# Kernel tuning notes

Measured on AMD Instinct MI355X. Metric: run time of the kernel, lower is better.

The kernel has to match this reference:

```python
import jax, jax.numpy as jnp
import numpy as np

EPS = 1e-5

def conv1x1(x, w):
    # x: (B,C,H,W), w: (O,C) -> (B,O,H,W)
    return jnp.einsum('bchw,oc->bohw', x, w)

def bn_relu(y, g, b, m, v):
    s = g / jnp.sqrt(v + EPS)
    return jax.nn.relu(y * s[None, :, None, None] + (b - m * s)[None, :, None, None])

def cbr(x, w, g, b, m, v):
    return bn_relu(conv1x1(x, w), g, b, m, v)

def _bn_params(key, c):
    k1, k2, k3, k4 = jax.random.split(key, 4)
    g = 1.0 + 0.1 * jax.random.normal(k1, (c,), jnp.float32)
    b = 0.1 * jax.random.normal(k2, (c,), jnp.float32)
    m = 0.05 * jax.random.normal(k3, (c,), jnp.float32)
    v = jax.random.uniform(k4, (c,), jnp.float32, 0.5, 1.5)
    return g, b, m, v

def setup_inputs() -> dict:
    key = jax.random.key(0)
    B, Cin, H, W = 8, 512, 64, 64
    Ck, Cv, Cout = 256, 256, 512
    ks = jax.random.split(key, 12)
    def w(k, o, c):
        return jax.random.normal(k, (o, c), jnp.float32) * (1.0 / np.sqrt(c))
    inp = {}
    inp['x'] = jax.random.normal(ks[0], (B, Cin, H, W), jnp.float32)
    # f_key
    inp['kW1'] = w(ks[1], Ck, Cin); inp['kG1'], inp['kB1'], inp['kM1'], inp['kV1'] = _bn_params(ks[2], Ck)
    inp['kW2'] = w(ks[3], Ck, Ck);  inp['kG2'], inp['kB2'], inp['kM2'], inp['kV2'] = _bn_params(ks[4], Ck)
    # f_query
    inp['qW1'] = w(ks[5], Ck, Cin); inp['qG1'], inp['qB1'], inp['qM1'], inp['qV1'] = _bn_params(ks[6], Ck)
    inp['qW2'] = w(ks[7], Ck, Ck);  inp['qG2'], inp['qB2'], inp['qM2'], inp['qV2'] = _bn_params(ks[8], Ck)
    # f_value
    inp['vW'] = w(ks[9], Cv, Cin)
    # W (output projection)
    inp['wW'] = w(ks[10], Cout, Cv); inp['wG'], inp['wB'], inp['wM'], inp['wV'] = _bn_params(ks[11], Cout)
    return inp

def reference(x,
              kW1, kG1, kB1, kM1, kV1, kW2, kG2, kB2, kM2, kV2,
              qW1, qG1, qB1, qM1, qV1, qW2, qG2, qB2, qM2, qV2,
              vW,
              wW, wG, wB, wM, wV):
    B, _, H, W = x.shape
    q = cbr(cbr(x, qW1, qG1, qB1, qM1, qV1), qW2, qG2, qB2, qM2, qV2)  # (B,Ck,H,W)
    k = cbr(cbr(x, kW1, kG1, kB1, kM1, kV1), kW2, kG2, kB2, kM2, kV2)  # (B,Ck,H,W)
    v = conv1x1(x, vW)                                                  # (B,Cv,H,W)
    Ck = q.shape[1]; Cv = v.shape[1]; N = H * W
    qf = q.reshape(B, Ck, N)   # query = qf^T -> (B,N,Ck)
    kf = k.reshape(B, Ck, N)
    vf = v.reshape(B, Cv, N)
    sim = jnp.einsum('bcn,bcm->bnm', qf, kf) * (Ck ** -0.5)  # (B,N,N)
    attn = jax.nn.softmax(sim, axis=-1)
    ctx = jnp.einsum('bnm,bcm->bcn', attn, vf).reshape(B, Cv, H, W)
    return cbr(ctx, wW, wG, wB, wM, wV)
```

## Files before the change

kernel.cpp:

```cpp
#include <hip/hip_runtime.h>
#include <hip/hip_bf16.h>

typedef __attribute__((ext_vector_type(8))) short bf16x8;
typedef __attribute__((ext_vector_type(4))) float f32x4;

#define MFMA16(a, b, c) __builtin_amdgcn_mfma_f32_16x16x32_bf16(a, b, c, 0, 0, 0)

static __device__ __forceinline__ unsigned short f2bf(float f) {
  union { __hip_bfloat16 h; unsigned short u; } cv;
  cv.h = __float2bfloat16(f);
  return cv.u;
}

static __device__ __forceinline__ void gload16(const void* gptr, void* lptr) {
  __builtin_amdgcn_global_load_lds(
      (const __attribute__((address_space(1))) void*)gptr,
      (__attribute__((address_space(3))) void*)lptr, 16, 0, 0);
}


__global__ void conv_w_k(const float* __restrict__ qW1, const float* __restrict__ kW1,
                         const float* __restrict__ qW2, const float* __restrict__ kW2,
                         const float* __restrict__ vW, const float* __restrict__ wW,
                         __hip_bfloat16* __restrict__ dst) {
  int i = blockIdx.x * 256 + threadIdx.x;
  const float* src; int off;
  if (i < 131072)      { src = qW1; off = i; }
  else if (i < 262144) { src = kW1; off = i - 131072; }
  else if (i < 327680) { src = qW2; off = i - 262144; }
  else if (i < 393216) { src = kW2; off = i - 327680; }
  else if (i < 524288) { src = vW;  off = i - 393216; }
  else                 { src = wW;  off = i - 524288; }
  dst[i] = __float2bfloat16(src[off]);
}

__global__ void bn_all_k(const float* __restrict__ qG1, const float* __restrict__ qB1, const float* __restrict__ qM1, const float* __restrict__ qV1,
                         const float* __restrict__ qG2, const float* __restrict__ qB2, const float* __restrict__ qM2, const float* __restrict__ qV2,
                         const float* __restrict__ kG1, const float* __restrict__ kB1, const float* __restrict__ kM1, const float* __restrict__ kV1,
                         const float* __restrict__ kG2, const float* __restrict__ kB2, const float* __restrict__ kM2, const float* __restrict__ kV2,
                         const float* __restrict__ wG, const float* __restrict__ wB, const float* __restrict__ wM, const float* __restrict__ wV,
                         float* __restrict__ base) {
  int bidx = blockIdx.x, tid = threadIdx.x;
  const float *g, *b, *m, *v; float *s, *t; int i;
  if (bidx == 0)      { g = qG1; b = qB1; m = qM1; v = qV1; s = base;        t = base + 256;  i = tid; }
  else if (bidx == 1) { g = qG2; b = qB2; m = qM2; v = qV2; s = base + 512;  t = base + 768;  i = tid; }
  else if (bidx == 2) { g = kG1; b = kB1; m = kM1; v = kV1; s = base + 1024; t = base + 1280; i = tid; }
  else if (bidx == 3) { g = kG2; b = kB2; m = kM2; v = kV2; s = base + 1536; t = base + 1792; i = tid; }
  else                { g = wG;  b = wB;  m = wM;  v = wV;  s = base + 2048; t = base + 2560; i = (bidx - 4) * 256 + tid; }
  float sv = g[i] * rsqrtf(v[i] + 1e-5f);
  s[i] = sv;
  t[i] = b[i] - m[i] * sv;
}

__global__ __launch_bounds__(256) void transpose_k(const float* __restrict__ x,
                                                   __hip_bfloat16* __restrict__ xT) {
  __shared__ float tile[64][65];
  const int n0 = blockIdx.x * 64, c0 = blockIdx.y * 64, b = blockIdx.z;
  const int tx = threadIdx.x, ty = threadIdx.y;
  const float* xp = x + ((size_t)(b * 512 + c0) * 4096) + n0;
#pragma unroll
  for (int i = 0; i < 16; ++i) {
    int c = ty + 4 * i;
    tile[c][tx] = xp[(size_t)c * 4096 + tx];
  }
  __syncthreads();
  __hip_bfloat16* op = xT + ((size_t)(b * 4096 + n0) * 512) + c0;
#pragma unroll
  for (int i = 0; i < 16; ++i) {
    int nl = ty + 4 * i;
    op[(size_t)nl * 512 + tx] = __float2bfloat16(tile[tx][nl]);
  }
}

template <int EPI>
__global__ __launch_bounds__(256) void gemm_nt_k(
    const __hip_bfloat16* __restrict__ A, long sA,
    const __hip_bfloat16* __restrict__ B, long sB,
    void* __restrict__ Cp, long sC,
    int lda, int ldb, int ldc, int K,
    const float* __restrict__ s, const float* __restrict__ t) {
  __shared__ short As[128][72];
  __shared__ short Bs[128][72];
  const int tid = threadIdx.x;
  const int w = tid >> 6, l = tid & 63, g = l >> 4, ln = l & 15;
  const int wr = w >> 1, wc = w & 1;
  const int rb = blockIdx.x * 128, cb = blockIdx.y * 128;
  const __hip_bfloat16* Ab = A + (size_t)blockIdx.z * sA;
  const __hip_bfloat16* Bb = B + (size_t)blockIdx.z * sB;

  f32x4 acc[4][4];
#pragma unroll
  for (int i = 0; i < 4; ++i)
#pragma unroll
    for (int j = 0; j < 4; ++j) acc[i][j] = (f32x4){0.f, 0.f, 0.f, 0.f};

  const int r0 = tid >> 3;
  const int c8 = (tid & 7) * 8;

  for (int k0 = 0; k0 < K; k0 += 64) {
#pragma unroll
    for (int i = 0; i < 4; ++i) {
      const int r = r0 + 32 * i;
      *(uint4*)&As[r][c8] = *(const uint4*)(Ab + (size_t)(rb + r) * lda + (k0 + c8));
      *(uint4*)&Bs[r][c8] = *(const uint4*)(Bb + (size_t)(cb + r) * ldb + (k0 + c8));
    }
    __syncthreads();
#pragma unroll
    for (int kk = 0; kk < 2; ++kk) {
      bf16x8 av[4], bv[4];
#pragma unroll
      for (int i = 0; i < 4; ++i) av[i] = *(const bf16x8*)&As[64 * wr + 16 * i + ln][32 * kk + 8 * g];
#pragma unroll
      for (int i = 0; i < 4; ++i) bv[i] = *(const bf16x8*)&Bs[64 * wc + 16 * i + ln][32 * kk + 8 * g];
#pragma unroll
      for (int mi = 0; mi < 4; ++mi)
#pragma unroll
        for (int ni = 0; ni < 4; ++ni)
          acc[mi][ni] = MFMA16(av[mi], bv[ni], acc[mi][ni]);
    }
    __syncthreads();
  }

  const int row0 = rb + 64 * wr + 4 * g;
  const int col0 = cb + 64 * wc + ln;

  if (EPI == 2) {
    float* C = (float*)Cp + (size_t)blockIdx.z * sC;
#pragma unroll
    for (int mi = 0; mi < 4; ++mi) {
#pragma unroll
      for (int r = 0; r < 4; ++r) {
        const int R = row0 + 16 * mi + r;
        const float sr = s[R], tr = t[R];
#pragma unroll
        for (int ni = 0; ni < 4; ++ni) {
          float v = fmaf(acc[mi][ni][r], sr, tr);
          C[(size_t)R * ldc + (col0 + 16 * ni)] = v > 0.f ? v : 0.f;
        }
      }
    }
  } else {
    __hip_bfloat16* C = (__hip_bfloat16*)Cp + (size_t)blockIdx.z * sC;
    float sc[4], tc[4];
    if (EPI == 1) {
#pragma unroll
      for (int ni = 0; ni < 4; ++ni) { sc[ni] = s[col0 + 16 * ni]; tc[ni] = t[col0 + 16 * ni]; }
    }
#pragma unroll
    for (int mi = 0; mi < 4; ++mi) {
#pragma unroll
      for (int ni = 0; ni < 4; ++ni) {
#pragma unroll
        for (int r = 0; r < 4; ++r) {
          float v = acc[mi][ni][r];
          if (EPI == 1) { v = fmaf(v, sc[ni], tc[ni]); v = v > 0.f ? v : 0.f; }
          C[(size_t)(row0 + 16 * mi + r) * ldc + (col0 + 16 * ni)] = __float2bfloat16(v);
        }
      }
    }
  }
}

__global__ __launch_bounds__(256, 2) void flash_k(
    const __hip_bfloat16* __restrict__ Q,
    const __hip_bfloat16* __restrict__ Kt,
    const __hip_bfloat16* __restrict__ V,
    __hip_bfloat16* __restrict__ O) {
  __shared__ short Ks[2][64 * 256];
  __shared__ short Ps[64 * 64];
  __shared__ float aLds[64];
  __shared__ float lLds[64];
  __shared__ int fLds[4];

  const int tid = threadIdx.x;
  const int w = tid >> 6, l = tid & 63, g = l >> 4, ln = l & 15;
  const int bid = blockIdx.x;
  const int batch = bid & 7;
  const int qb = (bid >> 3) << 6;
  const size_t bo = (size_t)batch * (4096 * 256);
  const float CE = 0.09016844005556021f;

  const int swz45 = (16 * g) ^ ((ln & 3) << 4);
  const int s6 = ((ln >> 2) & 1) << 6;
  const char* Ka0 = (const char*)Ks[0] + (ln * 512 + swz45 + s6);
  const char* Ka1 = Ka0 + (((ln >> 2) & 1) ? -64 : 64);
  const char* Kb0 = Ka0 + 32768;
  const char* Kb1 = Ka1 + 32768;
  const char* Pr0 = (const char*)Ps + (ln * 128 + swz45 + s6);
  const char* Pr1 = Pr0 + (((ln >> 2) & 1) ? -64 : 64);
  const int pwOff = (16 * w + ln) * 128 + 8 * (g & 1) + (((g >> 1) ^ (ln & 1)) << 4) +
                    (((ln >> 1) & 1) << 5) + s6;

  bf16x8 qf[8];
  {
    const __hip_bfloat16* qp = Q + bo + (size_t)(qb + 16 * w + ln) * 256 + 8 * g;
#pragma unroll
    for (int kk = 0; kk < 8; ++kk) qf[kk] = *(const bf16x8*)(qp + 32 * kk);
  }

  f32x4 acc[4][4];
#pragma unroll
  for (int qg = 0; qg < 4; ++qg)
#pragma unroll
    for (int ci = 0; ci < 4; ++ci) acc[qg][ci] = (f32x4){0.f, 0.f, 0.f, 0.f};
  float m_run = -1e30f, l_run = 0.f;

  const int kRow = 16 * w + (l >> 5);
  const int kChunk = (l & 31) ^ (l >> 5);
  const short* kPtr[8];
#pragma unroll
  for (int j = 0; j < 8; ++j)
    kPtr[j] = (const short*)(Kt + bo) + (size_t)(kRow + 2 * j) * 256 + 8 * (kChunk ^ ((2 * j) & 7));
  const short* vPtr[4];
#pragma unroll
  for (int ci = 0; ci < 4; ++ci)
    vPtr[ci] = (const short*)(V + bo) + (size_t)(64 * w + 16 * ci + ln) * 4096 + 8 * g;

  bf16x8 vfrA[8], vfrB[8];

#define STAGEK(NB)                                                     \
  do {                                                                 \
    _Pragma("unroll") for (int j = 0; j < 8; ++j) {                    \
      gload16(kPtr[j], (short*)Ks[NB] + w * 4096 + j * 512);           \
      kPtr[j] += 16384;                      \
    }                                                                  \
  } while (0)

#define ISSUEV(VARR)                                                   \
  do {                                                                 \
    _Pragma("unroll") for (int ci = 0; ci < 4; ++ci) {                 \
      asm volatile("global_load_dwordx4 %0, %2, off\n\t"               \
                   "global_load_dwordx4 %1, %2, off offset:64"         \
                   : "=&v"(VARR[2 * ci]), "=&v"(VARR[2 * ci + 1])      \
                   : "v"(vPtr[ci]));                                   \
      vPtr[ci] += 64;                  \
    }                                                                  \
  } while (0)

  STAGEK(0);
  __builtin_amdgcn_sched_barrier(0);
  ISSUEV(vfrA);
  __builtin_amdgcn_sched_barrier(0);

#define BODY(T, K0P, K1P, VCUR, VNXT, NB)                                      \
  do {                                                                         \
                      \
    asm volatile("s_waitcnt vmcnt(8)" ::: "memory");                           \
    __builtin_amdgcn_sched_barrier(0);                                         \
                                    \
    f32x4 sf[4];                                                               \
    _Pragma("unroll") for (int mi = 0; mi < 4; ++mi)                           \
        sf[mi] = (f32x4){0.f, 0.f, 0.f, 0.f};                                  \
    __builtin_amdgcn_s_setprio(1);                                             \
    _Pragma("unroll") for (int kk = 0; kk < 8; ++kk) {                         \
      const char* kp = ((kk & 1) ? K1P : K0P) + 128 * (kk >> 1);               \
      _Pragma("unroll") for (int mi = 0; mi < 4; ++mi) {                       \
        bf16x8 a = *(const bf16x8*)(kp + 8192 * mi);                           \
        sf[mi] = MFMA16(a, qf[kk], sf[mi]);                                    \
      }                                                                        \
    }                                                                          \
    __builtin_amdgcn_s_setprio(0);                                             \
    __builtin_amdgcn_sched_barrier(0);                                         \
    if ((T) < 63) {                                                            \
      STAGEK(NB);                               \
      __builtin_amdgcn_sched_barrier(0);                                       \
      ISSUEV(VNXT);                           \
      __builtin_amdgcn_sched_barrier(0);                                       \
    }                                                                          \
                                          \
    float sv[16];                                                              \
    _Pragma("unroll") for (int mi = 0; mi < 4; ++mi)                           \
        _Pragma("unroll") for (int r = 0; r < 4; ++r)                          \
        sv[4 * mi + r] = sf[mi][r];                                            \
    float a0 = fmaxf(fmaxf(sv[0], sv[1]), sv[2]);                              \
    float a1 = fmaxf(fmaxf(sv[3], sv[4]), sv[5]);                              \
    float a2 = fmaxf(fmaxf(sv[6], sv[7]), sv[8]);                              \
    float a3 = fmaxf(fmaxf(sv[9], sv[10]), sv[11]);                            \
    float a4 = fmaxf(fmaxf(sv[12], sv[13]), sv[14]);                           \
    float mmax = fmaxf(fmaxf(fmaxf(fmaxf(a0, a1), a2), fmaxf(a3, a4)), sv[15]);\
    mmax = fmaxf(mmax, __shfl_xor(mmax, 16));                                  \
    mmax = fmaxf(mmax, __shfl_xor(mmax, 32));                                  \
    float alpha = 1.0f;                                                        \
    int rs = 0;                                                                \
    if (!__all((mmax - m_run) * CE <= 8.0f)) {                                 \
      float m_new = fmaxf(m_run, mmax);                                        \
      alpha = exp2f((m_run - m_new) * CE);                                     \
      l_run *= alpha;                                                          \
      m_run = m_new;                                                           \
      rs = 1;                                                                  \
    }                                                                          \
    float p[16], psum = 0.f;                                                   \
    _Pragma("unroll") for (int j = 0; j < 16; ++j) {                           \
      p[j] = exp2f((sv[j] - m_run) * CE);                                      \
      psum += p[j];                                                            \
    }                                                                          \
    psum += __shfl_xor(psum, 16);                                              \
    psum += __shfl_xor(psum, 32);                                              \
    l_run += psum;                                                             \
    {                                                                          \
      uint2 pk0, pk1, pk2, pk3;                                                \
      pk0.x = (unsigned)f2bf(p[0]) | ((unsigned)f2bf(p[1]) << 16);             \
      pk0.y = (unsigned)f2bf(p[2]) | ((unsigned)f2bf(p[3]) << 16);             \
      pk1.x = (unsigned)f2bf(p[4]) | ((unsigned)f2bf(p[5]) << 16);             \
      pk1.y = (unsigned)f2bf(p[6]) | ((unsigned)f2bf(p[7]) << 16);             \
      pk2.x = (unsigned)f2bf(p[8]) | ((unsigned)f2bf(p[9]) << 16);             \
      pk2.y = (unsigned)f2bf(p[10]) | ((unsigned)f2bf(p[11]) << 16);           \
      pk3.x = (unsigned)f2bf(p[12]) | ((unsigned)f2bf(p[13]) << 16);           \
      pk3.y = (unsigned)f2bf(p[14]) | ((unsigned)f2bf(p[15]) << 16);           \
      char* Pb = (char*)Ps;                                                    \
      *(uint2*)(Pb + (pwOff ^ 0)) = pk0;                                       \
      *(uint2*)(Pb + (pwOff ^ 32)) = pk1;                                      \
      *(uint2*)(Pb + (pwOff ^ 64)) = pk2;                                      \
      *(uint2*)(Pb + (pwOff ^ 96)) = pk3;                                      \
    }                                                                          \
    if (g == 0) aLds[16 * w + ln] = alpha;                                     \
    if (l == 0) fLds[w] = rs;                                                  \
                                  \
    asm volatile("s_waitcnt lgkmcnt(0)" ::: "memory");                         \
    __builtin_amdgcn_sched_barrier(0);                                         \
    __builtin_amdgcn_s_barrier();                                              \
    asm volatile("" ::: "memory");                                             \
    __builtin_amdgcn_sched_barrier(0);                                         \
                              \
    {                                                                          \
      int4 fl = *(const int4*)fLds;                                            \
      if (fl.x | fl.y | fl.z | fl.w) {                                         \
        _Pragma("unroll") for (int qg = 0; qg < 4; ++qg) {                     \
          f32x4 av = *(const f32x4*)&aLds[16 * qg + 4 * g];                    \
          _Pragma("unroll") for (int ci = 0; ci < 4; ++ci) acc[qg][ci] *= av;  \
        }                                                                      \
      }                                                                        \
    }                                                                          \
                         \
    if ((T) < 63) {                                                            \
      asm volatile("s_waitcnt vmcnt(16)" ::: "memory");                        \
    } else {                                                                   \
      asm volatile("s_waitcnt vmcnt(0)" ::: "memory");                         \
    }                                                                          \
    __builtin_amdgcn_sched_barrier(0);                                         \
                              \
    __builtin_amdgcn_s_setprio(1);                                             \
    _Pragma("unroll") for (int kk = 0; kk < 2; ++kk) {                         \
      _Pragma("unroll") for (int qg = 0; qg < 4; ++qg) {                       \
        bf16x8 pa = *(const bf16x8*)((kk ? Pr1 : Pr0) + 2048 * qg);            \
        _Pragma("unroll") for (int ci = 0; ci < 4; ++ci)                       \
            acc[qg][ci] = MFMA16(pa, VCUR[2 * ci + kk], acc[qg][ci]);          \
      }                                                                        \
    }                                                                          \
    __builtin_amdgcn_s_setprio(0);                                             \
    __builtin_amdgcn_sched_barrier(0);                                         \
                   \
    __builtin_amdgcn_s_barrier();                                              \
    asm volatile("" ::: "memory");                                             \
    __builtin_amdgcn_sched_barrier(0);                                         \
  } while (0)

  for (int tp = 0; tp < 32; ++tp) {
    const int t0 = 2 * tp;
    BODY(t0, Ka0, Ka1, vfrA, vfrB, 1);
    BODY(t0 + 1, Kb0, Kb1, vfrB, vfrA, 0);
  }
#undef BODY
#undef STAGEK
#undef ISSUEV

  if (g == 0) lLds[16 * w + ln] = l_run;
  __syncthreads();

  __hip_bfloat16* Ob = O + bo;
#pragma unroll
  for (int qg = 0; qg < 4; ++qg) {
    f32x4 lv = *(const f32x4*)&lLds[16 * qg + 4 * g];
    f32x4 li;
#pragma unroll
    for (int r = 0; r < 4; ++r) li[r] = 1.0f / lv[r];
#pragma unroll
    for (int ci = 0; ci < 4; ++ci) {
#pragma unroll
      for (int r = 0; r < 4; ++r) {
        float val = acc[qg][ci][r] * li[r];
        Ob[(size_t)(qb + 16 * qg + 4 * g + r) * 256 + 64 * w + 16 * ci + ln] = __float2bfloat16(val);
      }
    }
  }
}


extern "C" void kernel_launch(void* const* d_in, const int* in_sizes, int n_in,
                              void* d_out, int out_size, void* d_ws, size_t ws_size,
                              hipStream_t stream) {
  const float* x   = (const float*)d_in[0];
  const float* kW1 = (const float*)d_in[1];
  const float* kG1 = (const float*)d_in[2];
  const float* kB1 = (const float*)d_in[3];
  const float* kM1 = (const float*)d_in[4];
  const float* kV1 = (const float*)d_in[5];
  const float* kW2 = (const float*)d_in[6];
  const float* kG2 = (const float*)d_in[7];
  const float* kB2 = (const float*)d_in[8];
  const float* kM2 = (const float*)d_in[9];
  const float* kV2 = (const float*)d_in[10];
  const float* qW1 = (const float*)d_in[11];
  const float* qG1 = (const float*)d_in[12];
  const float* qB1 = (const float*)d_in[13];
  const float* qM1 = (const float*)d_in[14];
  const float* qV1 = (const float*)d_in[15];
  const float* qW2 = (const float*)d_in[16];
  const float* qG2 = (const float*)d_in[17];
  const float* qB2 = (const float*)d_in[18];
  const float* qM2 = (const float*)d_in[19];
  const float* qV2 = (const float*)d_in[20];
  const float* vW  = (const float*)d_in[21];
  const float* wW  = (const float*)d_in[22];
  const float* wG  = (const float*)d_in[23];
  const float* wB  = (const float*)d_in[24];
  const float* wM  = (const float*)d_in[25];
  const float* wV  = (const float*)d_in[26];

  char* ws = (char*)d_ws;
  __hip_bfloat16* bQW1 = (__hip_bfloat16*)(ws + 0);
  __hip_bfloat16* bKW1 = (__hip_bfloat16*)(ws + 262144);
  __hip_bfloat16* bQW2 = (__hip_bfloat16*)(ws + 524288);
  __hip_bfloat16* bKW2 = (__hip_bfloat16*)(ws + 655360);
  __hip_bfloat16* bVW  = (__hip_bfloat16*)(ws + 786432);
  __hip_bfloat16* bWW  = (__hip_bfloat16*)(ws + 1048576);
  float* bnBase = (float*)(ws + 1310720);
  float* sQ1 = bnBase + 0;
  float* tQ1 = bnBase + 256;
  float* sQ2 = bnBase + 512;
  float* tQ2 = bnBase + 768;
  float* sK1 = bnBase + 1024;
  float* tK1 = bnBase + 1280;
  float* sK2 = bnBase + 1536;
  float* tK2 = bnBase + 1792;
  float* sWo = bnBase + 2048;
  float* tWo = bnBase + 2560;
  __hip_bfloat16* xT   = (__hip_bfloat16*)(ws + 2097152);
  __hip_bfloat16* bufA = (__hip_bfloat16*)(ws + 35651584);
  __hip_bfloat16* q2b  = (__hip_bfloat16*)(ws + 52428800);
  __hip_bfloat16* k2b  = (__hip_bfloat16*)(ws + 69206016);
  __hip_bfloat16* vB   = (__hip_bfloat16*)(ws + 85983232);

  conv_w_k<<<2560, 256, 0, stream>>>(qW1, kW1, qW2, kW2, vW, wW, bQW1);
  bn_all_k<<<6, 256, 0, stream>>>(qG1, qB1, qM1, qV1, qG2, qB2, qM2, qV2,
                                  kG1, kB1, kM1, kV1, kG2, kB2, kM2, kV2,
                                  wG, wB, wM, wV, bnBase);

  transpose_k<<<dim3(64, 8, 8), dim3(64, 4), 0, stream>>>(x, xT);

  gemm_nt_k<1><<<dim3(32, 2, 8), 256, 0, stream>>>(xT, 2097152L, bQW1, 0L, bufA, 1048576L,
                                                   512, 512, 256, 512, sQ1, tQ1);
  gemm_nt_k<1><<<dim3(32, 2, 8), 256, 0, stream>>>(bufA, 1048576L, bQW2, 0L, q2b, 1048576L,
                                                   256, 256, 256, 256, sQ2, tQ2);
  gemm_nt_k<1><<<dim3(32, 2, 8), 256, 0, stream>>>(xT, 2097152L, bKW1, 0L, bufA, 1048576L,
                                                   512, 512, 256, 512, sK1, tK1);
  gemm_nt_k<1><<<dim3(32, 2, 8), 256, 0, stream>>>(bufA, 1048576L, bKW2, 0L, k2b, 1048576L,
                                                   256, 256, 256, 256, sK2, tK2);
  gemm_nt_k<0><<<dim3(2, 32, 8), 256, 0, stream>>>(bVW, 0L, xT, 2097152L, vB, 1048576L,
                                                   512, 512, 4096, 512, nullptr, nullptr);
  flash_k<<<512, 256, 0, stream>>>(q2b, k2b, vB, bufA);
  gemm_nt_k<2><<<dim3(4, 32, 8), 256, 0, stream>>>(bWW, 0L, bufA, 1048576L, d_out, 2097152L,
                                                   256, 256, 4096, 256, sWo, tWo);
}
```

Measured before the change: 367.8 us.

## Software-pipeline flash attention: overlap QK of next tile with PV of current

Restructures the attention main loop into a skewed pipeline. Each iteration computes QK^T for tile T while running the PV product for tile T-1, with explicit prologue and epilogue. The V register fragments drop from double to single buffering, and V loads are issued after PV so they overlap softmax. This aims to hide softmax and LDS latency behind MFMA work and to cut register pressure, but it changes the wait counts and barrier placement, which risks stalls.

Result: faster. 305.0 us (-17.1%).

```diff
diff --git a/kernel.cpp b/kernel.cpp
--- a/kernel.cpp
+++ b/kernel.cpp
@@ -182,10 +182,10 @@
 
   const int swz45 = (16 * g) ^ ((ln & 3) << 4);
   const int s6 = ((ln >> 2) & 1) << 6;
-  const char* Ka0 = (const char*)Ks[0] + (ln * 512 + swz45 + s6);
-  const char* Ka1 = Ka0 + (((ln >> 2) & 1) ? -64 : 64);
-  const char* Kb0 = Ka0 + 32768;
-  const char* Kb1 = Ka1 + 32768;
+  const char* KA0 = (const char*)Ks[0] + (ln * 512 + swz45 + s6);
+  const char* KA1 = KA0 + (((ln >> 2) & 1) ? -64 : 64);
+  const char* KB0 = KA0 + 32768;
+  const char* KB1 = KA1 + 32768;
   const char* Pr0 = (const char*)Ps + (ln * 128 + swz45 + s6);
   const char* Pr1 = Pr0 + (((ln >> 2) & 1) ? -64 : 64);
   const int pwOff = (16 * w + ln) * 128 + 8 * (g & 1) + (((g >> 1) ^ (ln & 1)) << 4) +
@@ -204,70 +204,76 @@
 #pragma unroll
     for (int ci = 0; ci < 4; ++ci) acc[qg][ci] = (f32x4){0.f, 0.f, 0.f, 0.f};
   float m_run = -1e30f, l_run = 0.f;
+  f32x4 sf[4];
+  bf16x8 vfr[8];
 
   const int kRow = 16 * w + (l >> 5);
   const int kChunk = (l & 31) ^ (l >> 5);
-  const short* kPtr[8];
-#pragma unroll
-  for (int j = 0; j < 8; ++j)
-    kPtr[j] = (const short*)(Kt + bo) + (size_t)(kRow + 2 * j) * 256 + 8 * (kChunk ^ ((2 * j) & 7));
-  const short* vPtr[4];
-#pragma unroll
-  for (int ci = 0; ci < 4; ++ci)
-    vPtr[ci] = (const short*)(V + bo) + (size_t)(64 * w + 16 * ci + ln) * 4096 + 8 * g;
-
-  bf16x8 vfrA[8], vfrB[8];
-
-#define STAGEK(NB)                                                     \
-  do {                                                                 \
-    _Pragma("unroll") for (int j = 0; j < 8; ++j) {                    \
-      gload16(kPtr[j], (short*)Ks[NB] + w * 4096 + j * 512);           \
-      kPtr[j] += 16384;                      \
-    }                                                                  \
-  } while (0)
-
-#define ISSUEV(VARR)                                                   \
-  do {                                                                 \
-    _Pragma("unroll") for (int ci = 0; ci < 4; ++ci) {                 \
-      asm volatile("global_load_dwordx4 %0, %2, off\n\t"               \
-                   "global_load_dwordx4 %1, %2, off offset:64"         \
-                   : "=&v"(VARR[2 * ci]), "=&v"(VARR[2 * ci + 1])      \
-                   : "v"(vPtr[ci]));                                   \
-      vPtr[ci] += 64;                  \
-    }                                                                  \
-  } while (0)
-
-  STAGEK(0);
-  __builtin_amdgcn_sched_barrier(0);
-  ISSUEV(vfrA);
-  __builtin_amdgcn_sched_barrier(0);
-
-#define BODY(T, K0P, K1P, VCUR, VNXT, NB)                                      \
-  do {                                                                         \
-                      \
-    asm volatile("s_waitcnt vmcnt(8)" ::: "memory");                           \
-    __builtin_amdgcn_sched_barrier(0);                                         \
-                                    \
-    f32x4 sf[4];                                                               \
+  const short* Kb = (const short*)(Kt + bo);
+  const short* Vp = (const short*)(V + bo) + (size_t)(64 * w + ln) * 4096 + 8 * g;
+
+#define SB __builtin_amdgcn_sched_barrier(0)
+
+#define STAGEK(NB, M0)                                                         \
+  do {                                                                         \
+    _Pragma("unroll") for (int j = 0; j < 8; ++j) {                            \
+      const short* gp =                                                        \
+          Kb + (size_t)((M0) + kRow + 2 * j) * 256 + 8 * (kChunk ^ ((2 * j) & 7)); \
+      gload16(gp, (short*)Ks[NB] + w * 4096 + j * 512);                        \
+    }                                                                          \
+  } while (0)
+
+#define ISSUEV(M0)                                                             \
+  do {                                                                         \
+    _Pragma("unroll") for (int ci = 0; ci < 4; ++ci)                           \
+        _Pragma("unroll") for (int kk = 0; kk < 2; ++kk) {                     \
+      const short* gp = Vp + (size_t)ci * (16 * 4096) + ((M0) + 32 * kk);      \
+      asm volatile("global_load_dwordx4 %0, %1, off"                           \
+                   : "=v"(vfr[2 * ci + kk]) : "v"(gp));                        \
+    }                                                                          \
+  } while (0)
+
+#define QKP(K0P, K1P)                                                          \
+  do {                                                                         \
     _Pragma("unroll") for (int mi = 0; mi < 4; ++mi)                           \
         sf[mi] = (f32x4){0.f, 0.f, 0.f, 0.f};                                  \
     __builtin_amdgcn_s_setprio(1);                                             \
     _Pragma("unroll") for (int kk = 0; kk < 8; ++kk) {                         \
-      const char* kp = ((kk & 1) ? K1P : K0P) + 128 * (kk >> 1);               \
+      const char* kp = ((kk & 1) ? (K1P) : (K0P)) + 128 * (kk >> 1);           \
       _Pragma("unroll") for (int mi = 0; mi < 4; ++mi) {                       \
         bf16x8 a = *(const bf16x8*)(kp + 8192 * mi);                           \
         sf[mi] = MFMA16(a, qf[kk], sf[mi]);                                    \
       }                                                                        \
     }                                                                          \
     __builtin_amdgcn_s_setprio(0);                                             \
-    __builtin_amdgcn_sched_barrier(0);                                         \
-    if ((T) < 63) {                                                            \
-      STAGEK(NB);                               \
-      __builtin_amdgcn_sched_barrier(0);                                       \
-      ISSUEV(VNXT);                           \
-      __builtin_amdgcn_sched_barrier(0);                                       \
-    }                                                                          \
-                                          \
+  } while (0)
+
+#define RESCALE                                                                \
+  do {                                                                         \
+    int4 fl = *(const int4*)fLds;                                              \
+    if (fl.x | fl.y | fl.z | fl.w) {                                           \
+      _Pragma("unroll") for (int qg = 0; qg < 4; ++qg) {                       \
+        f32x4 av = *(const f32x4*)&aLds[16 * qg + 4 * g];                      \
+        _Pragma("unroll") for (int ci = 0; ci < 4; ++ci) acc[qg][ci] *= av;    \
+      }                                                                        \
+    }                                                                          \
+  } while (0)
+
+#define PVP                                                                    \
+  do {                                                                         \
+    __builtin_amdgcn_s_setprio(1);                                             \
+    _Pragma("unroll") for (int kk = 0; kk < 2; ++kk) {                         \
+      _Pragma("unroll") for (int qg = 0; qg < 4; ++qg) {                       \
+        bf16x8 pa = *(const bf16x8*)((kk ? Pr1 : Pr0) + 2048 * qg);            \
+        _Pragma("unroll") for (int ci = 0; ci < 4; ++ci)                       \
+            acc[qg][ci] = MFMA16(pa, vfr[2 * ci + kk], acc[qg][ci]);           \
+      }                                                                        \
+    }                                                                          \
+    __builtin_amdgcn_s_setprio(0);                                             \
+  } while (0)
+
+#define SOFTMAX                                                                \
+  do {                                                                         \
     float sv[16];                                                              \
     _Pragma("unroll") for (int mi = 0; mi < 4; ++mi)                           \
         _Pragma("unroll") for (int r = 0; r < 4; ++r)                          \
@@ -315,54 +321,73 @@
     }                                                                          \
     if (g == 0) aLds[16 * w + ln] = alpha;                                     \
     if (l == 0) fLds[w] = rs;                                                  \
-                                  \
+  } while (0)
+
+#define BODY(K0P, K1P, NB, T, DOSTAGE)                                         \
+  do {                                                                         \
+    QKP(K0P, K1P);                                                             \
+    SB;                                                                        \
+    if (DOSTAGE) STAGEK(NB, ((T) + 1) << 6);                                   \
+    SB;                                                                        \
+    RESCALE;                                                                   \
+    if (DOSTAGE) { asm volatile("s_waitcnt vmcnt(8)" ::: "memory"); }          \
+    else         { asm volatile("s_waitcnt vmcnt(0)" ::: "memory"); }          \
+    SB;                                                                        \
+    PVP;                                                                       \
+    SB;                                                                        \
+    ISSUEV((T) << 6);                                                          \
+    SB;                                                                        \
     asm volatile("s_waitcnt lgkmcnt(0)" ::: "memory");                         \
-    __builtin_amdgcn_sched_barrier(0);                                         \
-    __builtin_amdgcn_s_barrier();                                              \
+    SB;                                                                        \
+    __builtin_amdgcn_s_barrier();                  \
     asm volatile("" ::: "memory");                                             \
-    __builtin_amdgcn_sched_barrier(0);                                         \
-                              \
-    {                                                                          \
-      int4 fl = *(const int4*)fLds;                                            \
-      if (fl.x | fl.y | fl.z | fl.w) {                                         \
-        _Pragma("unroll") for (int qg = 0; qg < 4; ++qg) {                     \
-          f32x4 av = *(const f32x4*)&aLds[16 * qg + 4 * g];                    \
-          _Pragma("unroll") for (int ci = 0; ci < 4; ++ci) acc[qg][ci] *= av;  \
-        }                                                                      \
-      }                                                                        \
-    }                                                                          \
-                         \
-    if ((T) < 63) {                                                            \
-      asm volatile("s_waitcnt vmcnt(16)" ::: "memory");                        \
-    } else {                                                                   \
-      asm volatile("s_waitcnt vmcnt(0)" ::: "memory");                         \
-    }                                                                          \
-    __builtin_amdgcn_sched_barrier(0);                                         \
-                              \
-    __builtin_amdgcn_s_setprio(1);                                             \
-    _Pragma("unroll") for (int kk = 0; kk < 2; ++kk) {                         \
-      _Pragma("unroll") for (int qg = 0; qg < 4; ++qg) {                       \
-        bf16x8 pa = *(const bf16x8*)((kk ? Pr1 : Pr0) + 2048 * qg);            \
-        _Pragma("unroll") for (int ci = 0; ci < 4; ++ci)                       \
-            acc[qg][ci] = MFMA16(pa, VCUR[2 * ci + kk], acc[qg][ci]);          \
-      }                                                                        \
-    }                                                                          \
-    __builtin_amdgcn_s_setprio(0);                                             \
-    __builtin_amdgcn_sched_barrier(0);                                         \
-                   \
-    __builtin_amdgcn_s_barrier();                                              \
+    SB;                                                                        \
+    SOFTMAX;                                                                   \
+    asm volatile("s_waitcnt vmcnt(8) lgkmcnt(0)" ::: "memory");                \
+    SB;                                                                        \
+    __builtin_amdgcn_s_barrier();          \
     asm volatile("" ::: "memory");                                             \
-    __builtin_amdgcn_sched_barrier(0);                                         \
-  } while (0)
-
-  for (int tp = 0; tp < 32; ++tp) {
-    const int t0 = 2 * tp;
-    BODY(t0, Ka0, Ka1, vfrA, vfrB, 1);
-    BODY(t0 + 1, Kb0, Kb1, vfrB, vfrA, 0);
-  }
+    SB;                                                                        \
+  } while (0)
+
+  STAGEK(0, 0);
+  SB;
+  asm volatile("s_waitcnt vmcnt(0)" ::: "memory");
+  SB;
+  __builtin_amdgcn_s_barrier();
+  asm volatile("" ::: "memory");
+  SB;
+  QKP(KA0, KA1);
+  SB;
+  STAGEK(1, 64);
+  SB;
+  ISSUEV(0);
+  SB;
+  SOFTMAX;
+  asm volatile("s_waitcnt vmcnt(8) lgkmcnt(0)" ::: "memory");
+  SB;
+  __builtin_amdgcn_s_barrier();
+  asm volatile("" ::: "memory");
+  SB;
+
+  for (int m = 0; m < 31; ++m) {
+    BODY(KB0, KB1, 0, 2 * m + 1, 1);
+    BODY(KA0, KA1, 1, 2 * m + 2, 1);
+  }
+  BODY(KB0, KB1, 0, 63, 0);
+  RESCALE;
+  asm volatile("s_waitcnt vmcnt(0)" ::: "memory");
+  SB;
+  PVP;
+
 #undef BODY
+#undef SOFTMAX
+#undef PVP
+#undef RESCALE
+#undef QKP
+#undef ISSUEV
 #undef STAGEK
-#undef ISSUEV
+#undef SB
 
   if (g == 0) lLds[16 * w + ln] = l_run;
   __syncthreads();
```
